# Performance work log

Hardware: AMD Instinct MI355X
Metric: run time of the kernel (lower is better)

The kernel has to match this reference:

```python
import jax, jax.numpy as jnp
import numpy as np

ALPHA = 0.2  # LeakyReLU negative slope
NEG_INF = -9e15


def gat_layer(h, adj_mask, W, a, concat):
    # h: [N, F_in], W: [F_in, F_out], a: [2*F_out, 1]
    Wh = h @ W                                   # [N, F_out]
    f_out = W.shape[1]
    e1 = Wh @ a[:f_out]                          # [N, 1]
    e2 = Wh @ a[f_out:]                          # [N, 1]
    e = jax.nn.leaky_relu(e1 + e2.T, ALPHA)      # [N, N] pairwise scores
    att = jnp.where(adj_mask, e, NEG_INF)
    att = jax.nn.softmax(att, axis=1)            # masked row softmax
    h_prime = att @ Wh                           # [N, F_out] aggregate
    out = jax.nn.elu(h_prime) if concat else h_prime
    return out, att


def setup_inputs() -> dict:
    N, nfeat, nhid, nclass = 8192, 512, 256, 16
    key = jax.random.key(0)
    k = jax.random.split(key, 6)
    x = jax.random.normal(k[0], (N, nfeat), dtype=jnp.float32)
    adj = jax.random.randint(k[1], (N, N), 0, 2, dtype=jnp.int32)
    W1 = jax.random.normal(k[2], (nfeat, nhid), dtype=jnp.float32) * (1.0 / np.sqrt(nfeat))
    a1 = jax.random.normal(k[3], (2 * nhid, 1), dtype=jnp.float32) * 0.1
    W2 = jax.random.normal(k[4], (nhid, nclass), dtype=jnp.float32) * (1.0 / np.sqrt(nhid))
    a2 = jax.random.normal(k[5], (2 * nclass, 1), dtype=jnp.float32) * 0.1
    return {"x": x, "adj": adj, "W1": W1, "a1": a1, "W2": W2, "a2": a2}


def reference(x, adj, W1, a1, W2, a2):
    adj_mask = adj > 0
    # layer 1: attentions (concat=True -> ELU)
    h1, att1 = gat_layer(x, adj_mask, W1, a1, concat=True)
    # out layer (concat=False) + sigmoid
    h2, att2 = gat_layer(h1, adj_mask, W2, a2, concat=False)
    out = jax.nn.sigmoid(h2)
    # mirrors torch return: (x, gft_list, att_list, attention)
    return out, h1, att1, att2
```

## Files before the change

kernel.cpp:

```cpp
#include <hip/hip_runtime.h>
#include <hip/hip_bf16.h>

#define LRELU_ALPHA 0.2f

typedef __attribute__((ext_vector_type(8))) __bf16 bf16x8;
typedef __attribute__((ext_vector_type(4))) float f32x4;
typedef __attribute__((ext_vector_type(8))) unsigned short u16x8;
typedef __attribute__((ext_vector_type(4))) unsigned short u16x4;

__device__ __forceinline__ unsigned short f2bf(float f) {
  unsigned int u = __float_as_uint(f);
  u += 0x7fffu + ((u >> 16) & 1u);
  return (unsigned short)(u >> 16);
}

__global__ __launch_bounds__(256) void gemm_f32_k(
    const float* __restrict__ A, const float* __restrict__ B,
    float* __restrict__ C, int M, int K, int Ncols)
{
  __shared__ float As[128][17];
  __shared__ float Bs[16][65];
  int t = threadIdx.x;
  int row0 = blockIdx.x * 128;
  int col0 = blockIdx.y * 64;
  int ty = t >> 4, tx = t & 15;
  float acc[8][4];
#pragma unroll
  for (int i = 0; i < 8; ++i)
#pragma unroll
    for (int j = 0; j < 4; ++j) acc[i][j] = 0.f;

  for (int kt = 0; kt < K; kt += 16) {
    __syncthreads();
    {
      int r = t >> 1, h = t & 1;
      const float4* src = (const float4*)(A + (size_t)(row0 + r) * K + kt + h * 8);
      float4 v0 = src[0], v1 = src[1];
      float* dst = &As[r][h * 8];
      dst[0]=v0.x; dst[1]=v0.y; dst[2]=v0.z; dst[3]=v0.w;
      dst[4]=v1.x; dst[5]=v1.y; dst[6]=v1.z; dst[7]=v1.w;
    }
    {
      int kr = t >> 4, seg = t & 15;
      const float4* src = (const float4*)(B + (size_t)(kt + kr) * Ncols + col0 + seg * 4);
      float4 v = src[0];
      float* dst = &Bs[kr][seg * 4];
      dst[0]=v.x; dst[1]=v.y; dst[2]=v.z; dst[3]=v.w;
    }
    __syncthreads();
#pragma unroll
    for (int k = 0; k < 16; ++k) {
      float bb[4];
#pragma unroll
      for (int j = 0; j < 4; ++j) bb[j] = Bs[k][tx * 4 + j];
#pragma unroll
      for (int i = 0; i < 8; ++i) {
        float aa = As[ty * 8 + i][k];
#pragma unroll
        for (int j = 0; j < 4; ++j) acc[i][j] = fmaf(aa, bb[j], acc[i][j]);
      }
    }
  }
#pragma unroll
  for (int i = 0; i < 8; ++i) {
    float4 v = make_float4(acc[i][0], acc[i][1], acc[i][2], acc[i][3]);
    *(float4*)(C + (size_t)(row0 + ty * 8 + i) * Ncols + col0 + tx * 4) = v;
  }
}

__global__ __launch_bounds__(256) void calc_e_k(
    const float* __restrict__ Wh, const float* __restrict__ a,
    float* __restrict__ e1, float* __restrict__ e2, int F)
{
  int row = blockIdx.x * 4 + (threadIdx.x >> 6);
  int l = threadIdx.x & 63;
  const float* r = Wh + (size_t)row * F;
  float s1 = 0.f, s2 = 0.f;
  for (int f = l; f < F; f += 64) {
    float v = r[f];
    s1 += v * a[f];
    s2 += v * a[F + f];
  }
#pragma unroll
  for (int off = 32; off; off >>= 1) {
    s1 += __shfl_down(s1, off);
    s2 += __shfl_down(s2, off);
  }
  if (l == 0) { e1[row] = s1; e2[row] = s2; }
}

__global__ void transpose_bf16_k(const float* __restrict__ in, unsigned short* __restrict__ out,
                                 int R, int Cc)
{
  __shared__ float tile[32][33];
  int tx = threadIdx.x, ty = threadIdx.y;
  int c0 = blockIdx.x * 32, r0 = blockIdx.y * 32;
  int c = c0 + tx;
  if (c < Cc) {
    for (int i = ty; i < 32; i += 8)
      tile[i][tx] = in[(size_t)(r0 + i) * Cc + c];
  }
  __syncthreads();
  int r = r0 + tx;
  for (int i = ty; i < 32; i += 8) {
    int cc = c0 + i;
    if (cc < Cc)
      out[(size_t)cc * R + r] = f2bf(tile[tx][i]);
  }
}

__global__ __launch_bounds__(256) void att_softmax1_k(
    const int* __restrict__ adj, const float* __restrict__ e1,
    const float* __restrict__ e2, float* __restrict__ att,
    unsigned* __restrict__ bits)
{
  __shared__ float red[4];
  int i = blockIdx.x, t = threadIdx.x;
  const int4* arow = (const int4*)(adj + (size_t)i * 8192);
  unsigned* brow = bits + (size_t)i * 256;
  float e1i = e1[i];
  float4 vv[8];
  float s = 0.f;
#pragma unroll
  for (int it = 0; it < 8; ++it) {
    int j4 = t + it * 256;
    int4 a4 = arow[j4];
    float4 ev = *(const float4*)(e2 + j4 * 4);
    unsigned n = (unsigned)(a4.x > 0) | ((unsigned)(a4.y > 0) << 1)
               | ((unsigned)(a4.z > 0) << 2) | ((unsigned)(a4.w > 0) << 3);
    unsigned v = n << ((t & 7) * 4);
    v |= __shfl_xor(v, 1);
    v |= __shfl_xor(v, 2);
    v |= __shfl_xor(v, 4);
    if ((t & 7) == 0) brow[it * 32 + (t >> 3)] = v;
    float e, p0, p1, p2, p3;
    e = e1i + ev.x; e = e > 0.f ? e : LRELU_ALPHA * e; p0 = (a4.x > 0) ? __expf(e) : 0.f;
    e = e1i + ev.y; e = e > 0.f ? e : LRELU_ALPHA * e; p1 = (a4.y > 0) ? __expf(e) : 0.f;
    e = e1i + ev.z; e = e > 0.f ? e : LRELU_ALPHA * e; p2 = (a4.z > 0) ? __expf(e) : 0.f;
    e = e1i + ev.w; e = e > 0.f ? e : LRELU_ALPHA * e; p3 = (a4.w > 0) ? __expf(e) : 0.f;
    vv[it] = make_float4(p0, p1, p2, p3);
    s += (p0 + p1) + (p2 + p3);
  }
#pragma unroll
  for (int off = 32; off; off >>= 1) s += __shfl_xor(s, off);
  if ((t & 63) == 0) red[t >> 6] = s;
  __syncthreads();
  s = red[0] + red[1] + red[2] + red[3];
  float inv = 1.f / s;
  float4* orow = (float4*)(att + (size_t)i * 8192);
#pragma unroll
  for (int it = 0; it < 8; ++it) {
    float4 p = vv[it];
    p.x *= inv; p.y *= inv; p.z *= inv; p.w *= inv;
    orow[t + it * 256] = p;
  }
}

__global__ __launch_bounds__(256) void att_softmax2_k(
    const unsigned* __restrict__ bits, const float* __restrict__ e1,
    const float* __restrict__ e2, float* __restrict__ att)
{
  __shared__ unsigned bw[256];
  __shared__ float red[4];
  int i = blockIdx.x, t = threadIdx.x;
  bw[t] = bits[(size_t)i * 256 + t];
  float e1i = e1[i];
  __syncthreads();
  float4 vv[8];
  float s = 0.f;
#pragma unroll
  for (int it = 0; it < 8; ++it) {
    int j4 = t + it * 256;
    float4 ev = *(const float4*)(e2 + j4 * 4);
    unsigned wb = bw[j4 >> 3];
    int b0 = (j4 & 7) * 4;
    float e, p0, p1, p2, p3;
    e = e1i + ev.x; e = e > 0.f ? e : LRELU_ALPHA * e; p0 = ((wb >> (b0 + 0)) & 1) ? __expf(e) : 0.f;
    e = e1i + ev.y; e = e > 0.f ? e : LRELU_ALPHA * e; p1 = ((wb >> (b0 + 1)) & 1) ? __expf(e) : 0.f;
    e = e1i + ev.z; e = e > 0.f ? e : LRELU_ALPHA * e; p2 = ((wb >> (b0 + 2)) & 1) ? __expf(e) : 0.f;
    e = e1i + ev.w; e = e > 0.f ? e : LRELU_ALPHA * e; p3 = ((wb >> (b0 + 3)) & 1) ? __expf(e) : 0.f;
    vv[it] = make_float4(p0, p1, p2, p3);
    s += (p0 + p1) + (p2 + p3);
  }
#pragma unroll
  for (int off = 32; off; off >>= 1) s += __shfl_xor(s, off);
  if ((t & 63) == 0) red[t >> 6] = s;
  __syncthreads();
  s = red[0] + red[1] + red[2] + red[3];
  float inv = 1.f / s;
  float4* orow = (float4*)(att + (size_t)i * 8192);
#pragma unroll
  for (int it = 0; it < 8; ++it) {
    float4 p = vv[it];
    p.x *= inv; p.y *= inv; p.z *= inv; p.w *= inv;
    orow[t + it * 256] = p;
  }
}

template<int BN, int SPLITK, int EPI>
__global__ __launch_bounds__(256) void gemm_mfma_k(
    const float* __restrict__ A, const unsigned short* __restrict__ BT,
    float* __restrict__ Cout, int M, int K, int ldc)
{
  constexpr int BM = 64, BK = 64;
  constexpr int WN = (BN == 64) ? 2 : 1;
  constexpr int WM = 4 / WN;
  constexpr int WROWS = BM / WM;
  constexpr int WCOLS = BN / WN;
  constexpr int FM = WROWS / 16;
  constexpr int FN = WCOLS / 16;
  __shared__ __align__(16) char As[BM * BK * 2];
  __shared__ __align__(16) char Bs[BN * BK * 2];
  int t = threadIdx.x;
  int row0 = blockIdx.x * BM;
  int col0 = blockIdx.y * BN;
  int ktiles = K / BK;
  int kt0 = blockIdx.z * (ktiles / SPLITK);
  int kt1 = kt0 + ktiles / SPLITK;
  int w = t >> 6, l = t & 63;
  int wm = w / WN, wn = w % WN;

  f32x4 acc[FM][FN] = {};

  int ar = t >> 2, aseg = t & 3;
  int swzA = (ar & 7) << 4;

  for (int kt = kt0; kt < kt1; ++kt) {
    __syncthreads();
    {
      const float4* src = (const float4*)(A + (size_t)(row0 + ar) * K + kt * BK + aseg * 16);
      float4 v0 = src[0], v1 = src[1], v2 = src[2], v3 = src[3];
      u16x8 c0, c1;
      c0[0]=f2bf(v0.x); c0[1]=f2bf(v0.y); c0[2]=f2bf(v0.z); c0[3]=f2bf(v0.w);
      c0[4]=f2bf(v1.x); c0[5]=f2bf(v1.y); c0[6]=f2bf(v1.z); c0[7]=f2bf(v1.w);
      c1[0]=f2bf(v2.x); c1[1]=f2bf(v2.y); c1[2]=f2bf(v2.z); c1[3]=f2bf(v2.w);
      c1[4]=f2bf(v3.x); c1[5]=f2bf(v3.y); c1[6]=f2bf(v3.z); c1[7]=f2bf(v3.w);
      int base = ar * 128 + aseg * 32;
      *(u16x8*)(As + ((base) ^ swzA)) = c0;
      *(u16x8*)(As + ((base + 16) ^ swzA)) = c1;
    }
    if (BN == 64) {
      int br = t >> 2, seg = t & 3;
      const u16x8* src = (const u16x8*)(BT + (size_t)(col0 + br) * K + kt * BK + seg * 16);
      u16x8 b0 = src[0], b1 = src[1];
      int base = br * 128 + seg * 32;
      int swz = (br & 7) << 4;
      *(u16x8*)(Bs + ((base) ^ swz)) = b0;
      *(u16x8*)(Bs + ((base + 16) ^ swz)) = b1;
    } else {
      int br = t >> 4, seg = t & 15;
      const u16x4* src = (const u16x4*)(BT + (size_t)(col0 + br) * K + kt * BK + seg * 4);
      u16x4 b0 = src[0];
      int base = br * 128 + seg * 8;
      int swz = (br & 7) << 4;
      *(u16x4*)(Bs + (base ^ swz)) = b0;
    }
    __syncthreads();
#pragma unroll
    for (int kk = 0; kk < BK; kk += 32) {
      bf16x8 af[FM], bfr[FN];
      int kb = (kk + (l >> 4) * 8) * 2;
#pragma unroll
      for (int fm = 0; fm < FM; ++fm) {
        int r = wm * WROWS + fm * 16 + (l & 15);
        af[fm] = *(const bf16x8*)(As + ((r * 128 + kb) ^ ((r & 7) << 4)));
      }
#pragma unroll
      for (int fn = 0; fn < FN; ++fn) {
        int c = wn * WCOLS + fn * 16 + (l & 15);
        bfr[fn] = *(const bf16x8*)(Bs + ((c * 128 + kb) ^ ((c & 7) << 4)));
      }
#pragma unroll
      for (int fm = 0; fm < FM; ++fm)
#pragma unroll
        for (int fn = 0; fn < FN; ++fn)
          acc[fm][fn] = __builtin_amdgcn_mfma_f32_16x16x32_bf16(af[fm], bfr[fn], acc[fm][fn], 0, 0, 0);
    }
  }
#pragma unroll
  for (int fm = 0; fm < FM; ++fm) {
#pragma unroll
    for (int fn = 0; fn < FN; ++fn) {
#pragma unroll
      for (int r = 0; r < 4; ++r) {
        int grow = row0 + wm * WROWS + fm * 16 + (l >> 4) * 4 + r;
        int gcol = col0 + wn * WCOLS + fn * 16 + (l & 15);
        float v = acc[fm][fn][r];
        if (EPI == 1) v = v > 0.f ? v : expm1f(v);
        size_t idx = (SPLITK > 1)
          ? ((size_t)blockIdx.z * M + grow) * ldc + gcol
          : (size_t)grow * ldc + gcol;
        Cout[idx] = v;
      }
    }
  }
}

__global__ __launch_bounds__(256) void gemm_small_k(
    const float* __restrict__ A, const float* __restrict__ B,
    float* __restrict__ C, int K, int Ncols)
{
  int t = threadIdx.x;
  int r = blockIdx.x * 16 + (t >> 4);
  int c = t & 15;
  const float* arow = A + (size_t)r * K;
  float acc = 0.f;
#pragma unroll 8
  for (int k = 0; k < K; ++k)
    acc = fmaf(arow[k], B[k * Ncols + c], acc);
  C[(size_t)r * Ncols + c] = acc;
}

__global__ void reduce_elu_k(const float* __restrict__ part, float* __restrict__ out, int total)
{
  int i = blockIdx.x * 256 + threadIdx.x;
  if (i < total) {
    float s = (part[i] + part[total + i]) + (part[2 * (size_t)total + i] + part[3 * (size_t)total + i]);
    out[i] = s > 0.f ? s : expm1f(s);
  }
}

__global__ void reduce_sig_k(const float* __restrict__ part, float* __restrict__ out, int total)
{
  int i = blockIdx.x * 256 + threadIdx.x;
  if (i < total) {
    float s = part[i] + part[total + i] + part[2 * (size_t)total + i] + part[3 * (size_t)total + i];
    out[i] = 1.f / (1.f + __expf(-s));
  }
}

extern "C" void kernel_launch(void* const* d_in, const int* in_sizes, int n_in,
                              void* d_out, int out_size, void* d_ws, size_t ws_size,
                              hipStream_t stream)
{
  const float* x   = (const float*)d_in[0];
  const int*   adj = (const int*)d_in[1];
  const float* W1  = (const float*)d_in[2];
  const float* a1  = (const float*)d_in[3];
  const float* W2  = (const float*)d_in[4];
  const float* a2  = (const float*)d_in[5];

  float* out  = (float*)d_out;
  float* h1   = out + 131072;
  float* att1 = h1 + 2097152;
  float* att2 = att1 + 67108864;

  float* ws = (float*)d_ws;
  float* wh1 = ws;
  unsigned short* bt1 = (unsigned short*)(wh1 + 2097152);
  float* e1a = wh1 + 2097152 + 1048576;
  float* e2a = e1a + 8192;
  float* wh2 = e2a + 8192;
  unsigned short* bt2 = (unsigned short*)(wh2 + 131072);
  float* e1b = wh2 + 131072 + 65536;
  float* e2b = e1b + 8192;
  float* part2 = e2b + 8192;
  unsigned* bits = (unsigned*)(part2 + 524288);
  float* part1 = (float*)(bits + 2097152);

  gemm_f32_k<<<dim3(64, 4), 256, 0, stream>>>(x, W1, wh1, 8192, 512, 256);
  calc_e_k<<<2048, 256, 0, stream>>>(wh1, a1, e1a, e2a, 256);
  transpose_bf16_k<<<dim3(8, 256), dim3(32, 8), 0, stream>>>(wh1, bt1, 8192, 256);
  att_softmax1_k<<<8192, 256, 0, stream>>>(adj, e1a, e2a, att1, bits);
  gemm_mfma_k<64, 4, 0><<<dim3(128, 4, 4), 256, 0, stream>>>(att1, bt1, part1, 8192, 8192, 256);
  reduce_elu_k<<<8192, 256, 0, stream>>>(part1, h1, 2097152);

  gemm_small_k<<<512, 256, 0, stream>>>(h1, W2, wh2, 256, 16);
  calc_e_k<<<2048, 256, 0, stream>>>(wh2, a2, e1b, e2b, 16);
  transpose_bf16_k<<<dim3(1, 256), dim3(32, 8), 0, stream>>>(wh2, bt2, 8192, 16);
  att_softmax2_k<<<8192, 256, 0, stream>>>(bits, e1b, e2b, att2);
  gemm_mfma_k<16, 4, 0><<<dim3(128, 1, 4), 256, 0, stream>>>(att2, bt2, part2, 8192, 8192, 16);
  reduce_sig_k<<<512, 256, 0, stream>>>(part2, out, 131072);
}
```

Baseline: 460.1 us.

## Emit bf16 copy of attention in softmax and feed bf16 GEMM

The layer-1 softmax now also writes a bf16 copy of the attention matrix, and a new MFMA GEMM reads that copy directly instead of loading the fp32 att1 and converting it. Each GEMM pass over the 8192x8192 matrix then moves half the bytes, with 4 column blocks re-reading A. The cost is an extra 128MB write from the softmax kernel, which can offset the saved reads.

```diff
diff --git a/kernel.cpp b/kernel.cpp
--- a/kernel.cpp
+++ b/kernel.cpp
@@ -112,7 +112,7 @@
 __global__ __launch_bounds__(256) void att_softmax1_k(
     const int* __restrict__ adj, const float* __restrict__ e1,
     const float* __restrict__ e2, float* __restrict__ att,
-    unsigned* __restrict__ bits)
+    unsigned short* __restrict__ attb, unsigned* __restrict__ bits)
 {
   __shared__ float red[4];
   int i = blockIdx.x, t = threadIdx.x;
@@ -148,11 +148,16 @@
   s = red[0] + red[1] + red[2] + red[3];
   float inv = 1.f / s;
   float4* orow = (float4*)(att + (size_t)i * 8192);
+  unsigned short* obrow = attb + (size_t)i * 8192;
 #pragma unroll
   for (int it = 0; it < 8; ++it) {
+    int j4 = t + it * 256;
     float4 p = vv[it];
     p.x *= inv; p.y *= inv; p.z *= inv; p.w *= inv;
-    orow[t + it * 256] = p;
+    orow[j4] = p;
+    u16x4 b;
+    b[0] = f2bf(p.x); b[1] = f2bf(p.y); b[2] = f2bf(p.z); b[3] = f2bf(p.w);
+    *(u16x4*)(obrow + j4 * 4) = b;
   }
 }
 
@@ -194,6 +199,82 @@
     float4 p = vv[it];
     p.x *= inv; p.y *= inv; p.z *= inv; p.w *= inv;
     orow[t + it * 256] = p;
+  }
+}
+
+__global__ __launch_bounds__(256) void gemm_mfma1b_k(
+    const unsigned short* __restrict__ A,
+    const unsigned short* __restrict__ BT,
+    float* __restrict__ part)
+{
+  constexpr int BM = 64, BN = 64, BK = 64;
+  __shared__ __align__(16) char As[BM * 128];
+  __shared__ __align__(16) char Bs[BN * 128];
+  int t = threadIdx.x;
+  int row0 = blockIdx.x * BM;
+  int col0 = blockIdx.y * BN;
+  int z = blockIdx.z;
+  int kt0 = z * 32, kt1 = kt0 + 32;
+  int w = t >> 6, l = t & 63;
+  int wm = w >> 1, wn = w & 1;
+
+  f32x4 acc[2][2] = {};
+
+  int ar = t >> 2, aseg = t & 3;
+  int swzA = (ar & 7) << 4;
+  const unsigned short* agp = A + (size_t)(row0 + ar) * 8192 + aseg * 16;
+
+  for (int kt = kt0; kt < kt1; ++kt) {
+    __syncthreads();
+    {
+      const u16x8* src = (const u16x8*)(agp + kt * BK);
+      u16x8 c0 = src[0], c1 = src[1];
+      int base = ar * 128 + aseg * 32;
+      *(u16x8*)(As + ((base) ^ swzA)) = c0;
+      *(u16x8*)(As + ((base + 16) ^ swzA)) = c1;
+    }
+    {
+      int br = t >> 2, seg = t & 3;
+      const u16x8* src = (const u16x8*)(BT + (size_t)(col0 + br) * 8192 + kt * BK + seg * 16);
+      u16x8 b0 = src[0], b1 = src[1];
+      int base = br * 128 + seg * 32;
+      int swz = (br & 7) << 4;
+      *(u16x8*)(Bs + ((base) ^ swz)) = b0;
+      *(u16x8*)(Bs + ((base + 16) ^ swz)) = b1;
+    }
+    __syncthreads();
+#pragma unroll
+    for (int kk = 0; kk < BK; kk += 32) {
+      bf16x8 af[2], bfr[2];
+      int kb = (kk + (l >> 4) * 8) * 2;
+#pragma unroll
+      for (int fm = 0; fm < 2; ++fm) {
+        int r = wm * 32 + fm * 16 + (l & 15);
+        af[fm] = *(const bf16x8*)(As + ((r * 128 + kb) ^ ((r & 7) << 4)));
+      }
+#pragma unroll
+      for (int fn = 0; fn < 2; ++fn) {
+        int c = wn * 32 + fn * 16 + (l & 15);
+        bfr[fn] = *(const bf16x8*)(Bs + ((c * 128 + kb) ^ ((c & 7) << 4)));
+      }
+#pragma unroll
+      for (int fm = 0; fm < 2; ++fm)
+#pragma unroll
+        for (int fn = 0; fn < 2; ++fn)
+          acc[fm][fn] = __builtin_amdgcn_mfma_f32_16x16x32_bf16(af[fm], bfr[fn], acc[fm][fn], 0, 0, 0);
+    }
+  }
+#pragma unroll
+  for (int fm = 0; fm < 2; ++fm) {
+#pragma unroll
+    for (int fn = 0; fn < 2; ++fn) {
+#pragma unroll
+      for (int r = 0; r < 4; ++r) {
+        int grow = row0 + wm * 32 + fm * 16 + (l >> 4) * 4 + r;
+        int gcol = col0 + wn * 32 + fn * 16 + (l & 15);
+        part[((size_t)z * 8192 + grow) * 256 + gcol] = acc[fm][fn][r];
+      }
+    }
   }
 }
 
@@ -357,12 +438,13 @@
   float* part2 = e2b + 8192;
   unsigned* bits = (unsigned*)(part2 + 524288);
   float* part1 = (float*)(bits + 2097152);
+  unsigned short* att1b = (unsigned short*)(part1 + 8388608);
 
   gemm_f32_k<<<dim3(64, 4), 256, 0, stream>>>(x, W1, wh1, 8192, 512, 256);
   calc_e_k<<<2048, 256, 0, stream>>>(wh1, a1, e1a, e2a, 256);
   transpose_bf16_k<<<dim3(8, 256), dim3(32, 8), 0, stream>>>(wh1, bt1, 8192, 256);
-  att_softmax1_k<<<8192, 256, 0, stream>>>(adj, e1a, e2a, att1, bits);
-  gemm_mfma_k<64, 4, 0><<<dim3(128, 4, 4), 256, 0, stream>>>(att1, bt1, part1, 8192, 8192, 256);
+  att_softmax1_k<<<8192, 256, 0, stream>>>(adj, e1a, e2a, att1, att1b, bits);
+  gemm_mfma1b_k<<<dim3(128, 4, 4), 256, 0, stream>>>(att1b, bt1, part1);
   reduce_elu_k<<<8192, 256, 0, stream>>>(part1, h1, 2097152);
 
   gemm_small_k<<<512, 256, 0, stream>>>(h1, W2, wh2, 256, 16);
```

Result: faster. 440.3 us (-4.3%).
